# Kernel optimization log

Hardware: AMD Instinct MI355X
Metric: run time of the kernel (lower is better)

Reference implementation:

```python
import jax, jax.numpy as jnp
import numpy as np

N, E, DIN, DOUT = 100000, 500000, 256, 1


def setup_inputs() -> dict:
    key = jax.random.key(0)
    k1, k2, k3, k4 = jax.random.split(key, 4)
    x = jax.random.normal(k1, (N, DIN), dtype=jnp.float32)
    edge_label_index = jax.random.randint(k2, (2, E), 0, N, dtype=jnp.int64)
    # nn.Linear default init: U(-1/sqrt(fan_in), 1/sqrt(fan_in)); plain scaled normal is fine for a numeric reference
    W1 = jax.random.normal(k3, (2 * DIN, DIN), dtype=jnp.float32) / np.sqrt(2 * DIN)
    b1 = jnp.zeros((DIN,), dtype=jnp.float32)
    W2 = jax.random.normal(k4, (DIN, DOUT), dtype=jnp.float32) / np.sqrt(DIN)
    b2 = jnp.zeros((DOUT,), dtype=jnp.float32)
    return {"x": x, "edge_label_index": edge_label_index, "W1": W1, "b1": b1, "W2": W2, "b2": b2}


def reference(x, edge_label_index, W1, b1, W2, b2):
    x_i = x[edge_label_index[0]]            # [E, DIN] gather src
    x_j = x[edge_label_index[1]]            # [E, DIN] gather dst
    h = jnp.concatenate([x_i, x_j], axis=-1)  # [E, 2*DIN]
    h = jax.nn.relu(h @ W1 + b1)            # [E, DIN]
    return h @ W2 + b2                      # [E, DOUT]
```

## Files before the change

### kernel.cpp

```cpp
#include <hip/hip_runtime.h>
#include <hip/hip_bf16.h>


typedef short short8 __attribute__((ext_vector_type(8)));
typedef float f32x4 __attribute__((ext_vector_type(4)));

#define DINC 256
#define NOUTC 512

__device__ inline unsigned short f2bf(float f) {
  union { float f; unsigned u; } c; c.f = f;
  unsigned u = c.u;
  return (unsigned short)((u + 0x7FFFu + ((u >> 16) & 1u)) >> 16);
}
__device__ inline float bf2f(unsigned short h) {
  union { unsigned u; float f; } c; c.u = ((unsigned)h) << 16;
  return c.f;
}

__global__ void w1t_kernel(const float* __restrict__ W1, unsigned short* __restrict__ W1t) {
  int t = blockIdx.x * 256 + threadIdx.x;
  int j = t >> 8, k = t & 255;
  float v = W1[(size_t)(k + ((j >= 256) ? 256 : 0)) * DINC + (j & 255)];
  int sk = (((k >> 3) ^ (j & 7)) << 3) | (k & 7);
  W1t[(size_t)j * DINC + sk] = f2bf(v);
}

__global__ __launch_bounds__(256) void uv_gemm(const float* __restrict__ x,
                                               const unsigned short* __restrict__ W1t,
                                               unsigned short* __restrict__ uv,
                                               int Nn, int m_tiles) {
  __shared__ unsigned short As[2][128 * 64];
  __shared__ unsigned short Bs[2][128 * 64];

  int nwg = gridDim.x;
  int q = nwg >> 3, r = nwg & 7;
  int xcd = blockIdx.x & 7, rank = blockIdx.x >> 3;
  int L = (xcd < r) ? (xcd * (q + 1) + rank) : (r * (q + 1) + (xcd - r) * q + rank);
  int bm = L >> 2, bn = L & 3;

  int tid = threadIdx.x, lane = tid & 63, w = tid >> 6;
  int wm = w >> 1, wn = w & 1;
  int lr = lane & 15, kg = lane >> 4;
  int m0 = bm * 128 + wm * 64, n0 = bn * 128 + wn * 64;

  int arow = tid >> 4, ac4 = tid & 15;

  f32x4 acc[4][4] = {};
  float4 ar[8];

#define ISSUE_A(KT)                                                            \
  {                                                                            \
    _Pragma("unroll")                                                          \
    for (int j = 0; j < 8; ++j) {                                              \
      int grow = bm * 128 + j * 16 + arow;                                     \
      if (grow >= Nn) grow = Nn - 1;                                           \
      ar[j] = *((const float4*)(x + (size_t)grow * DINC + (KT) * 64) + ac4);   \
    }                                                                          \
  }

#define ISSUE_B(KT, BUF)                                                       \
  {                                                                            \
    _Pragma("unroll")                                                          \
    for (int c = 0; c < 4; ++c) {                                              \
      const unsigned short* src =                                              \
          W1t + (size_t)(bn * 128 + ((c * 256 + tid) >> 3)) * DINC +           \
          (KT) * 64 + (tid & 7) * 8;                                           \
      unsigned short* dst = &Bs[BUF][(c * 256 + w * 64) * 8];                  \
      __builtin_amdgcn_global_load_lds(                                        \
          (const __attribute__((address_space(1))) void*)src,                  \
          (__attribute__((address_space(3))) void*)dst, 16, 0, 0);             \
    }                                                                          \
  }

#define WRITE_A(BUF)                                                           \
  {                                                                            \
    _Pragma("unroll")                                                          \
    for (int j = 0; j < 8; ++j) {                                              \
      int rl = j * 16 + arow;                                                  \
      ushort4 pk;                                                              \
      pk.x = f2bf(ar[j].x); pk.y = f2bf(ar[j].y);                              \
      pk.z = f2bf(ar[j].z); pk.w = f2bf(ar[j].w);                              \
      char* dp = (char*)&As[BUF][0] + rl * 128 +                               \
                 ((((ac4 >> 1) ^ (rl & 7)) << 4) | ((ac4 & 1) << 3));          \
      *(ushort4*)dp = pk;                                                      \
    }                                                                          \
  }

  ISSUE_A(0);
  ISSUE_B(0, 0);
  WRITE_A(0);
  __syncthreads();

  for (int kt = 0; kt < 4; ++kt) {
    int b = kt & 1;
    if (kt < 3) { ISSUE_A(kt + 1); ISSUE_B(kt + 1, b ^ 1); }

#pragma unroll
    for (int ks = 0; ks < 2; ++ks) {
      short8 af[4], bf_[4];
#pragma unroll
      for (int mf = 0; mf < 4; ++mf) {
        int row = wm * 64 + mf * 16 + lr;
        int phys = (ks * 4 + kg) ^ (lr & 7);
        af[mf] = *(const short8*)((char*)&As[b][0] + row * 128 + phys * 16);
      }
#pragma unroll
      for (int nf = 0; nf < 4; ++nf) {
        int col = wn * 64 + nf * 16 + lr;
        int phys = (ks * 4 + kg) ^ (lr & 7);
        bf_[nf] = *(const short8*)((char*)&Bs[b][0] + col * 128 + phys * 16);
      }
#pragma unroll
      for (int mf = 0; mf < 4; ++mf)
#pragma unroll
        for (int nf = 0; nf < 4; ++nf)
          acc[mf][nf] = __builtin_amdgcn_mfma_f32_16x16x32_bf16(bf_[nf], af[mf],
                                                                acc[mf][nf], 0, 0, 0);
    }

    if (kt < 3) { WRITE_A(b ^ 1); }
    __syncthreads();
  }

#pragma unroll
  for (int mf = 0; mf < 4; ++mf) {
    int m = m0 + mf * 16 + lr;
    if (m < Nn) {
      unsigned short* orow = uv + (size_t)m * NOUTC;
#pragma unroll
      for (int nf = 0; nf < 4; ++nf) {
        ushort4 pk;
        pk.x = f2bf(acc[mf][nf][0]);
        pk.y = f2bf(acc[mf][nf][1]);
        pk.z = f2bf(acc[mf][nf][2]);
        pk.w = f2bf(acc[mf][nf][3]);
        *(ushort4*)(orow + n0 + nf * 16 + kg * 4) = pk;
      }
    }
  }
#undef ISSUE_A
#undef ISSUE_B
#undef WRITE_A
}

__global__ __launch_bounds__(256) void edge_kernel(const int* __restrict__ eliW,
                                                   const unsigned short* __restrict__ uv,
                                                   const float* __restrict__ b1,
                                                   const float* __restrict__ W2,
                                                   const float* __restrict__ b2,
                                                   float* __restrict__ out, int E) {
  int tid = threadIdx.x;
  int ql = tid & 15;
  bool is64 = ((eliW[1] | eliW[3] | eliW[5] | eliW[7] | eliW[9] | eliW[11]) == 0);
  int shift = is64 ? 1 : 0;

  float bl[16], wl[16];
  *(float4*)(bl + 0)  = *(const float4*)(b1 + ql * 8);
  *(float4*)(bl + 4)  = *(const float4*)(b1 + ql * 8 + 4);
  *(float4*)(bl + 8)  = *(const float4*)(b1 + 128 + ql * 8);
  *(float4*)(bl + 12) = *(const float4*)(b1 + 128 + ql * 8 + 4);
  *(float4*)(wl + 0)  = *(const float4*)(W2 + ql * 8);
  *(float4*)(wl + 4)  = *(const float4*)(W2 + ql * 8 + 4);
  *(float4*)(wl + 8)  = *(const float4*)(W2 + 128 + ql * 8);
  *(float4*)(wl + 12) = *(const float4*)(W2 + 128 + ql * 8 + 4);
  float bias2 = b2[0];

  int qid = (blockIdx.x * blockDim.x + tid) >> 4;
  int nq = (gridDim.x * blockDim.x) >> 4;

  for (int e = qid; e < E; e += nq) {
    int src = eliW[((size_t)e) << shift];
    int dst = eliW[((size_t)(E + e)) << shift];
    const unsigned short* up = uv + (size_t)src * NOUTC;
    const unsigned short* vp = uv + (size_t)dst * NOUTC + DINC;
    short8 uu[2], vv[2];
    uu[0] = *(const short8*)(up + ql * 8);
    uu[1] = *(const short8*)(up + 128 + ql * 8);
    vv[0] = *(const short8*)(vp + ql * 8);
    vv[1] = *(const short8*)(vp + 128 + ql * 8);
    float s = 0.f;
#pragma unroll
    for (int g = 0; g < 2; ++g)
#pragma unroll
      for (int j = 0; j < 8; ++j) {
        float h = bf2f((unsigned short)uu[g][j]) + bf2f((unsigned short)vv[g][j]) + bl[g * 8 + j];
        s += fmaxf(h, 0.f) * wl[g * 8 + j];
      }
#pragma unroll
    for (int off = 8; off; off >>= 1) s += __shfl_xor(s, off, 64);
    if (ql == 0) out[e] = s + bias2;
  }
}

extern "C" void kernel_launch(void* const* d_in, const int* in_sizes, int n_in,
                              void* d_out, int out_size, void* d_ws, size_t ws_size,
                              hipStream_t stream) {
  const float* x   = (const float*)d_in[0];
  const int*   eli = (const int*)d_in[1];
  const float* W1  = (const float*)d_in[2];
  const float* b1  = (const float*)d_in[3];
  const float* W2  = (const float*)d_in[4];
  const float* b2  = (const float*)d_in[5];
  float* out = (float*)d_out;

  int Nn = in_sizes[0] / DINC;
  int E  = in_sizes[1] / 2;

  unsigned short* W1t = (unsigned short*)d_ws;
  unsigned short* uv  = W1t + (size_t)NOUTC * DINC;

  w1t_kernel<<<512, 256, 0, stream>>>(W1, W1t);

  int m_tiles = (Nn + 127) / 128;
  uv_gemm<<<m_tiles * (NOUTC / 128), 256, 0, stream>>>(x, W1t, uv, Nn, m_tiles);

  edge_kernel<<<2048, 256, 0, stream>>>(eli, uv, b1, W2, b2, out, E);
}
```

Baseline: 145.4 us.

## Load W1 fragments directly into registers and use 8 waves per GEMM block

```diff
diff --git a/kernel.cpp b/kernel.cpp
--- a/kernel.cpp
+++ b/kernel.cpp
@@ -22,16 +22,14 @@
   int t = blockIdx.x * 256 + threadIdx.x;
   int j = t >> 8, k = t & 255;
   float v = W1[(size_t)(k + ((j >= 256) ? 256 : 0)) * DINC + (j & 255)];
-  int sk = (((k >> 3) ^ (j & 7)) << 3) | (k & 7);
-  W1t[(size_t)j * DINC + sk] = f2bf(v);
-}
-
-__global__ __launch_bounds__(256) void uv_gemm(const float* __restrict__ x,
-                                               const unsigned short* __restrict__ W1t,
-                                               unsigned short* __restrict__ uv,
-                                               int Nn, int m_tiles) {
+  W1t[(size_t)j * DINC + k] = f2bf(v);
+}
+
+__global__ __launch_bounds__(512, 4) void uv_gemm(const float* __restrict__ x,
+                                                  const unsigned short* __restrict__ W1t,
+                                                  unsigned short* __restrict__ uv,
+                                                  int Nn, int m_tiles) {
   __shared__ unsigned short As[2][128 * 64];
-  __shared__ unsigned short Bs[2][128 * 64];
 
   int nwg = gridDim.x;
   int q = nwg >> 3, r = nwg & 7;
@@ -40,65 +38,65 @@
   int bm = L >> 2, bn = L & 3;
 
   int tid = threadIdx.x, lane = tid & 63, w = tid >> 6;
-  int wm = w >> 1, wn = w & 1;
+  int wm = w >> 2, wn = w & 3;
   int lr = lane & 15, kg = lane >> 4;
-  int m0 = bm * 128 + wm * 64, n0 = bn * 128 + wn * 64;
-
-  int arow = tid >> 4, ac4 = tid & 15;
-
-  f32x4 acc[4][4] = {};
-  float4 ar[8];
+  int m0 = bm * 128 + wm * 64;
+  int n0 = bn * 128 + wn * 32;
+
+  int c4 = tid & 15, rb = tid >> 4;
+
+  f32x4 acc[4][2] = {};
+  float4 ar[4];
+  short8 breg[2][4];
 
 #define ISSUE_A(KT)                                                            \
   {                                                                            \
     _Pragma("unroll")                                                          \
-    for (int j = 0; j < 8; ++j) {                                              \
-      int grow = bm * 128 + j * 16 + arow;                                     \
+    for (int j = 0; j < 4; ++j) {                                              \
+      int grow = bm * 128 + j * 32 + rb;                                       \
       if (grow >= Nn) grow = Nn - 1;                                           \
-      ar[j] = *((const float4*)(x + (size_t)grow * DINC + (KT) * 64) + ac4);   \
+      ar[j] = *((const float4*)(x + (size_t)grow * DINC + (KT) * 64) + c4);    \
     }                                                                          \
   }
 
-#define ISSUE_B(KT, BUF)                                                       \
+#define LOAD_B(KT, BUF)                                                        \
   {                                                                            \
     _Pragma("unroll")                                                          \
-    for (int c = 0; c < 4; ++c) {                                              \
-      const unsigned short* src =                                              \
-          W1t + (size_t)(bn * 128 + ((c * 256 + tid) >> 3)) * DINC +           \
-          (KT) * 64 + (tid & 7) * 8;                                           \
-      unsigned short* dst = &Bs[BUF][(c * 256 + w * 64) * 8];                  \
-      __builtin_amdgcn_global_load_lds(                                        \
-          (const __attribute__((address_space(1))) void*)src,                  \
-          (__attribute__((address_space(3))) void*)dst, 16, 0, 0);             \
-    }                                                                          \
+    for (int ks = 0; ks < 2; ++ks)                                             \
+      _Pragma("unroll")                                                        \
+      for (int nf = 0; nf < 2; ++nf)                                           \
+        breg[BUF][ks * 2 + nf] = *(const short8*)(                             \
+            W1t + (size_t)(n0 + nf * 16 + lr) * DINC +                         \
+            (KT) * 64 + ks * 32 + kg * 8);                                     \
   }
 
 #define WRITE_A(BUF)                                                           \
   {                                                                            \
     _Pragma("unroll")                                                          \
-    for (int j = 0; j < 8; ++j) {                                              \
-      int rl = j * 16 + arow;                                                  \
+    for (int j = 0; j < 4; ++j) {                                              \
+      int rl = j * 32 + rb;                                                    \
       ushort4 pk;                                                              \
       pk.x = f2bf(ar[j].x); pk.y = f2bf(ar[j].y);                              \
       pk.z = f2bf(ar[j].z); pk.w = f2bf(ar[j].w);                              \
       char* dp = (char*)&As[BUF][0] + rl * 128 +                               \
-                 ((((ac4 >> 1) ^ (rl & 7)) << 4) | ((ac4 & 1) << 3));          \
+                 ((((c4 >> 1) ^ (rl & 7)) << 4) | ((c4 & 1) << 3));            \
       *(ushort4*)dp = pk;                                                      \
     }                                                                          \
   }
 
   ISSUE_A(0);
-  ISSUE_B(0, 0);
+  LOAD_B(0, 0);
   WRITE_A(0);
   __syncthreads();
 
+#pragma unroll
   for (int kt = 0; kt < 4; ++kt) {
-    int b = kt & 1;
-    if (kt < 3) { ISSUE_A(kt + 1); ISSUE_B(kt + 1, b ^ 1); }
+    const int b = kt & 1;
+    if (kt < 3) { ISSUE_A(kt + 1); LOAD_B(kt + 1, b ^ 1); }
 
 #pragma unroll
     for (int ks = 0; ks < 2; ++ks) {
-      short8 af[4], bf_[4];
+      short8 af[4];
 #pragma unroll
       for (int mf = 0; mf < 4; ++mf) {
         int row = wm * 64 + mf * 16 + lr;
@@ -106,21 +104,14 @@
         af[mf] = *(const short8*)((char*)&As[b][0] + row * 128 + phys * 16);
       }
 #pragma unroll
-      for (int nf = 0; nf < 4; ++nf) {
-        int col = wn * 64 + nf * 16 + lr;
-        int phys = (ks * 4 + kg) ^ (lr & 7);
-        bf_[nf] = *(const short8*)((char*)&Bs[b][0] + col * 128 + phys * 16);
-      }
-#pragma unroll
       for (int mf = 0; mf < 4; ++mf)
 #pragma unroll
-        for (int nf = 0; nf < 4; ++nf)
-          acc[mf][nf] = __builtin_amdgcn_mfma_f32_16x16x32_bf16(bf_[nf], af[mf],
-                                                                acc[mf][nf], 0, 0, 0);
+        for (int nf = 0; nf < 2; ++nf)
+          acc[mf][nf] = __builtin_amdgcn_mfma_f32_16x16x32_bf16(
+              breg[b][ks * 2 + nf], af[mf], acc[mf][nf], 0, 0, 0);
     }
 
-    if (kt < 3) { WRITE_A(b ^ 1); }
-    __syncthreads();
+    if (kt < 3) { WRITE_A(b ^ 1); __syncthreads(); }
   }
 
 #pragma unroll
@@ -129,7 +120,7 @@
     if (m < Nn) {
       unsigned short* orow = uv + (size_t)m * NOUTC;
 #pragma unroll
-      for (int nf = 0; nf < 4; ++nf) {
+      for (int nf = 0; nf < 2; ++nf) {
         ushort4 pk;
         pk.x = f2bf(acc[mf][nf][0]);
         pk.y = f2bf(acc[mf][nf][1]);
@@ -140,7 +131,7 @@
     }
   }
 #undef ISSUE_A
-#undef ISSUE_B
+#undef LOAD_B
 #undef WRITE_A
 }
 
@@ -213,7 +204,7 @@
   w1t_kernel<<<512, 256, 0, stream>>>(W1, W1t);
 
   int m_tiles = (Nn + 127) / 128;
-  uv_gemm<<<m_tiles * (NOUTC / 128), 256, 0, stream>>>(x, W1t, uv, Nn, m_tiles);
+  uv_gemm<<<m_tiles * (NOUTC / 128), 512, 0, stream>>>(x, W1t, uv, Nn, m_tiles);
 
   edge_kernel<<<2048, 256, 0, stream>>>(eli, uv, b1, W2, b2, out, E);
 }
```

Result: slower. 164.0 us (+12.8%).
